# Optimization experiments

Measured on AMD Instinct MI355X. Metric: run time of the kernel, lower is better.

Reference implementation:

```python
import jax, jax.numpy as jnp
import numpy as np

B, A, HR = 2, 180, 512
H_OUT = W_OUT = 512


def setup_inputs() -> dict:
    key = jax.random.key(0)
    k1, = jax.random.split(key, 1)
    sino = jax.random.normal(k1, (B, A, HR), dtype=jnp.float32)
    angles_deg = jnp.linspace(0.0, 180.0, A, endpoint=False, dtype=jnp.float32)
    return {"sino": sino, "angles_deg": angles_deg, "H": H_OUT, "W": W_OUT}


def _forward(sino, angles_deg, H, W):
    Bn, An, Hr = sino.shape
    pad = int(1.0 * 0.1 * min(H, W))  # pad_ratio = 1.0
    Hp, Wp = H + 2 * pad, W + 2 * pad

    # --- F.interpolate bilinear, align_corners=False: (A,B,Hr,1) -> (A,B,Hp,Wp).
    # Input width is 1, so width interp replicates the single column; only height interp matters.
    src = jnp.clip((jnp.arange(Hp, dtype=jnp.float32) + 0.5) * (Hr / Hp) - 0.5, 0.0, Hr - 1)
    i0 = jnp.floor(src).astype(jnp.int32)
    i1 = jnp.minimum(i0 + 1, Hr - 1)
    wH = src - i0.astype(jnp.float32)
    p = jnp.transpose(sino, (1, 0, 2)).astype(jnp.float32)  # (A,B,Hr)
    col = p[:, :, i0] * (1.0 - wH) + p[:, :, i1] * wH       # (A,B,Hp)
    proj = jnp.broadcast_to(col[:, :, :, None], (An, Bn, Hp, Wp))  # (A,B,Hp,Wp)

    # --- affine_grid (align_corners=False), sign = -1
    th = -jnp.deg2rad(angles_deg)
    c, s = jnp.cos(th), jnp.sin(th)                          # (A,)
    xs = (jnp.arange(Wp, dtype=jnp.float32) + 0.5) * (2.0 / Wp) - 1.0
    ys = (jnp.arange(Hp, dtype=jnp.float32) + 0.5) * (2.0 / Hp) - 1.0
    gx = c[:, None, None] * xs[None, None, :] - s[:, None, None] * ys[None, :, None]  # (A,Hp,Wp)
    gy = s[:, None, None] * xs[None, None, :] + c[:, None, None] * ys[None, :, None]

    # --- grid_sample bilinear, zeros padding, align_corners=False
    ix = ((gx + 1.0) * Wp - 1.0) * 0.5
    iy = ((gy + 1.0) * Hp - 1.0) * 0.5
    x0 = jnp.floor(ix).astype(jnp.int32); x1 = x0 + 1
    y0 = jnp.floor(iy).astype(jnp.int32); y1 = y0 + 1
    wx = ix - x0.astype(jnp.float32)
    wy = iy - y0.astype(jnp.float32)

    def corner(img, xi, yi, w):  # img (B,Hp,Wp); idx/w (Hp,Wp)
        valid = (xi >= 0) & (xi <= Wp - 1) & (yi >= 0) & (yi <= Hp - 1)
        xc = jnp.clip(xi, 0, Wp - 1)
        yc = jnp.clip(yi, 0, Hp - 1)
        return img[:, yc, xc] * (w * valid.astype(jnp.float32))[None]

    def sample(img, x0a, x1a, y0a, y1a, wxa, wya):
        return (corner(img, x0a, y0a, (1 - wxa) * (1 - wya)) +
                corner(img, x1a, y0a, wxa * (1 - wya)) +
                corner(img, x0a, y1a, (1 - wxa) * wya) +
                corner(img, x1a, y1a, wxa * wya))

    xr = jax.vmap(sample)(proj, x0, x1, y0, y1, wx, wy)      # (A,B,Hp,Wp)
    acc = xr.sum(axis=0) / (An + 1e-06)                      # (B,Hp,Wp)
    acc = acc[:, None, :, :]                                 # (B,1,Hp,Wp)
    if pad > 0:
        acc = acc[:, :, pad:Hp - pad, pad:Wp - pad]
    return acc


def reference(sino, angles_deg, H, W):
    return _forward(sino, angles_deg, H, W)
```

## Files before the change

### kernel.cpp

```cpp
#include <hip/hip_runtime.h>
#include <math.h>

#define B_N   2
#define A_N   180
#define HR_N  512
#define H_OUT 512
#define W_OUT 512
#define PAD   51
#define HP    614
#define WP    614
#define GUARD 64
#define HPP   (HP + 2*GUARD)
#define NPIX  (H_OUT * W_OUT)
#define HALF_A (A_N / 2)


__device__ __forceinline__ float col_val(const float* __restrict__ sino,
                                         int b, int a, int yy) {
    if (yy < 0 || yy >= HP) return 0.0f;
    float src = ((float)yy + 0.5f) * ((float)HR_N / (float)HP) - 0.5f;
    src = fminf(fmaxf(src, 0.0f), (float)(HR_N - 1));
    int i0 = (int)floorf(src);
    int i1 = min(i0 + 1, HR_N - 1);
    float wH = src - (float)i0;
    const float* srow = sino + ((size_t)b * A_N + a) * HR_N;
    return srow[i0] * (1.0f - wH) + srow[i1] * wH;
}

__global__ void prep_kernel(const float* __restrict__ sino,
                            const float* __restrict__ angles,
                            float4* __restrict__ pk,
                            float* __restrict__ tg) {
    int idx = blockIdx.x * blockDim.x + threadIdx.x;
    if (idx < A_N) {
        float th = -angles[idx] * (float)(M_PI / 180.0);
        tg[2 * idx]     = cosf(th);
        tg[2 * idx + 1] = sinf(th);
    }
    const int total = A_N * HPP;
    if (idx < total) {
        int y = idx % HPP;
        int a = idx / HPP;
        int yy = y - GUARD;
        float4 v;
        v.x = col_val(sino, 0, a, yy);
        v.y = col_val(sino, 1, a, yy);
        v.z = col_val(sino, 0, a, yy + 1);
        v.w = col_val(sino, 1, a, yy + 1);
        pk[idx] = v;
    }
}

__global__ __launch_bounds__(256) void bp_kernel(const float4* __restrict__ pk,
                                                 const float* __restrict__ tg,
                                                 float* __restrict__ out) {
    __shared__ float s_tg[2 * HALF_A];
    int t = threadIdx.x;
    int half = blockIdx.y;
    if (t < 2 * HALF_A) s_tg[t] = tg[half * (2 * HALF_A) + t];
    __syncthreads();

    int idx = blockIdx.x * blockDim.x + t;
    int w = idx & (W_OUT - 1);
    int h = idx >> 9;
    float X = (float)w - 255.5f;
    float Y = (float)h - 255.5f;

    float acc0 = 0.0f, acc1 = 0.0f;

    const float4* pkh = pk + (size_t)(half * HALF_A) * HPP + GUARD;

#pragma unroll 6
    for (int a = 0; a < HALF_A; ++a) {
        float c = s_tg[2 * a];
        float s = s_tg[2 * a + 1];
        float ix = fmaf(c, X, fmaf(-s, Y, 306.5f));
        float iy = fmaf(s, X, fmaf(c, Y, 306.5f));

        float xfac = fminf(fmaxf(ix + 1.0f, 0.0f), 1.0f)
                   * fminf(fmaxf((float)WP - ix, 0.0f), 1.0f);

        float y0f = floorf(iy);
        float wy  = iy - y0f;
        int   y0  = (int)y0f;

        float4 cv = pkh[(size_t)a * HPP + y0];
        acc0 = fmaf(xfac, fmaf(wy, cv.z - cv.x, cv.x), acc0);
        acc1 = fmaf(xfac, fmaf(wy, cv.w - cv.y, cv.y), acc1);
    }

    const float inv = 1.0f / (180.0f + 1e-6f);
    atomicAdd(&out[idx],        acc0 * inv);
    atomicAdd(&out[NPIX + idx], acc1 * inv);
}

extern "C" void kernel_launch(void* const* d_in, const int* in_sizes, int n_in,
                              void* d_out, int out_size, void* d_ws, size_t ws_size,
                              hipStream_t stream) {
    const float* sino   = (const float*)d_in[0];
    const float* angles = (const float*)d_in[1];
    float* ws   = (float*)d_ws;
    float4* pk  = (float4*)ws;
    float* tg   = ws + (size_t)4 * A_N * HPP;

    const int total = A_N * HPP;
    prep_kernel<<<(total + 255) / 256, 256, 0, stream>>>(sino, angles, pk, tg);

    hipMemsetAsync(d_out, 0, (size_t)out_size * sizeof(float), stream);

    dim3 grid(NPIX / 256, 2);
    bp_kernel<<<grid, 256, 0, stream>>>(pk, tg, (float*)d_out);
}
```

Before: 89.99 us.

## Tile backprojection into 16x16 pixel blocks with per-angle shared-memory detector windows

Switches from 1D row-strip blocks split by angle halves to 16x16 2D pixel tiles that process all 180 angles. For each chunk of 30 angles, the detector samples each tile needs are staged into a 24-entry shared-memory window per angle, so the inner loop reads LDS instead of scattered global float4s. Since each block now covers all angles, the output is written directly, which removes the memset and the atomics. The cost is more __syncthreads and fewer total blocks. Correctness relies on the window of 24 and the guard of 80 being wide enough for the footprint of a rotated tile.

```diff
diff --git a/kernel.cpp b/kernel.cpp
--- a/kernel.cpp
+++ b/kernel.cpp
@@ -9,10 +9,14 @@
 #define PAD   51
 #define HP    614
 #define WP    614
-#define GUARD 64
+#define GUARD 80
 #define HPP   (HP + 2*GUARD)
 #define NPIX  (H_OUT * W_OUT)
-#define HALF_A (A_N / 2)
+
+#define TILE   16
+#define CH     30
+#define NCH    (A_N / CH)
+#define WIN    24
 
 
 __device__ __forceinline__ float col_val(const float* __restrict__ sino,
@@ -54,44 +58,70 @@
 __global__ __launch_bounds__(256) void bp_kernel(const float4* __restrict__ pk,
                                                  const float* __restrict__ tg,
                                                  float* __restrict__ out) {
-    __shared__ float s_tg[2 * HALF_A];
-    int t = threadIdx.x;
-    int half = blockIdx.y;
-    if (t < 2 * HALF_A) s_tg[t] = tg[half * (2 * HALF_A) + t];
-    __syncthreads();
+    __shared__ float4 s_ang[A_N];
+    __shared__ int    s_base[A_N];
+    __shared__ float4 s_win[CH * WIN];
 
-    int idx = blockIdx.x * blockDim.x + t;
-    int w = idx & (W_OUT - 1);
-    int h = idx >> 9;
+    int t  = threadIdx.x;
+    int tx = blockIdx.x, ty = blockIdx.y;
+
+    if (t < A_N) {
+        float c = tg[2 * t];
+        float s = tg[2 * t + 1];
+        float Xc = (float)(tx * TILE) - 248.0f;
+        float Yc = (float)(ty * TILE) - 248.0f;
+        float iyc = fmaf(s, Xc, fmaf(c, Yc, 306.5f));
+        int base = (int)floorf(iyc) - 11;
+        s_ang[t]  = make_float4(c, s, (float)base, 0.0f);
+        s_base[t] = base;
+    }
+
+    int lx = t & (TILE - 1);
+    int ly = t >> 4;
+    int w = tx * TILE + lx;
+    int h = ty * TILE + ly;
     float X = (float)w - 255.5f;
     float Y = (float)h - 255.5f;
 
     float acc0 = 0.0f, acc1 = 0.0f;
+    __syncthreads();
 
-    const float4* pkh = pk + (size_t)(half * HALF_A) * HPP + GUARD;
+    for (int ch = 0; ch < NCH; ++ch) {
+        int a0 = ch * CH;
+        for (int e = t; e < CH * WIN; e += 256) {
+            int la = e / WIN;
+            int j  = e - la * WIN;
+            int a  = a0 + la;
+            int yy = s_base[a] + j + GUARD;
+            s_win[e] = pk[(size_t)a * HPP + yy];
+        }
+        __syncthreads();
 
 #pragma unroll 6
-    for (int a = 0; a < HALF_A; ++a) {
-        float c = s_tg[2 * a];
-        float s = s_tg[2 * a + 1];
-        float ix = fmaf(c, X, fmaf(-s, Y, 306.5f));
-        float iy = fmaf(s, X, fmaf(c, Y, 306.5f));
+        for (int la = 0; la < CH; ++la) {
+            float4 ang = s_ang[a0 + la];
+            float c = ang.x, s = ang.y, fb = ang.z;
+            float ix = fmaf(c, X, fmaf(-s, Y, 306.5f));
+            float iy = fmaf(s, X, fmaf(c, Y, 306.5f));
 
-        float xfac = fminf(fmaxf(ix + 1.0f, 0.0f), 1.0f)
-                   * fminf(fmaxf((float)WP - ix, 0.0f), 1.0f);
+            float xfac = fminf(fmaxf(ix + 1.0f, 0.0f), 1.0f)
+                       * fminf(fmaxf((float)WP - ix, 0.0f), 1.0f);
 
-        float y0f = floorf(iy);
-        float wy  = iy - y0f;
-        int   y0  = (int)y0f;
+            float f  = iy - fb;
+            int   li = (int)f;
+            float wy = f - (float)li;
 
-        float4 cv = pkh[(size_t)a * HPP + y0];
-        acc0 = fmaf(xfac, fmaf(wy, cv.z - cv.x, cv.x), acc0);
-        acc1 = fmaf(xfac, fmaf(wy, cv.w - cv.y, cv.y), acc1);
+            float4 cv = s_win[la * WIN + li];
+            acc0 = fmaf(xfac, fmaf(wy, cv.z - cv.x, cv.x), acc0);
+            acc1 = fmaf(xfac, fmaf(wy, cv.w - cv.y, cv.y), acc1);
+        }
+        __syncthreads();
     }
 
     const float inv = 1.0f / (180.0f + 1e-6f);
-    atomicAdd(&out[idx],        acc0 * inv);
-    atomicAdd(&out[NPIX + idx], acc1 * inv);
+    int idx = h * W_OUT + w;
+    out[idx]        = acc0 * inv;
+    out[NPIX + idx] = acc1 * inv;
 }
 
 extern "C" void kernel_launch(void* const* d_in, const int* in_sizes, int n_in,
@@ -106,8 +136,6 @@
     const int total = A_N * HPP;
     prep_kernel<<<(total + 255) / 256, 256, 0, stream>>>(sino, angles, pk, tg);
 
-    hipMemsetAsync(d_out, 0, (size_t)out_size * sizeof(float), stream);
-
-    dim3 grid(NPIX / 256, 2);
+    dim3 grid(W_OUT / TILE, H_OUT / TILE);
     bp_kernel<<<grid, 256, 0, stream>>>(pk, tg, (float*)d_out);
 }
```

New measurement: 87.25 us. 1.03x faster.
